# Kernel tuning notes

Hardware: AMD Instinct MI355X
Metric: run time of the kernel (lower is better)

## Reference

```python
import jax, jax.numpy as jnp
import numpy as np

DIM = 512
NUM_HEADS = 8
DIM_HEAD = DIM // NUM_HEADS


def _xavier(key, shape):
    fan_in, fan_out = shape[0], shape[1]
    a = (6.0 / (fan_in + fan_out)) ** 0.5
    return jax.random.uniform(key, shape, jnp.float32, -a, a)


def setup_inputs() -> dict:
    key = jax.random.key(0)
    ks = jax.random.split(key, 8)
    B, N, M = 2, 2048, 2048
    x = jax.random.normal(ks[0], (B, N, DIM), jnp.float32)
    source = jax.random.normal(ks[1], (B, M, DIM), jnp.float32)
    source_mask = jax.random.randint(ks[2], (B, M), 0, 2) > 0
    Wq = _xavier(ks[3], (DIM, DIM)); bq = jnp.zeros((DIM,), jnp.float32)
    Wk = _xavier(ks[4], (DIM, DIM)); bk = jnp.zeros((DIM,), jnp.float32)
    Wv = _xavier(ks[5], (DIM, DIM)); bv = jnp.zeros((DIM,), jnp.float32)
    Wm = _xavier(ks[6], (DIM, DIM)); bm = jnp.zeros((DIM,), jnp.float32)
    return {"x": x, "source": source, "source_mask": source_mask,
            "Wq": Wq, "bq": bq, "Wk": Wk, "bk": bk,
            "Wv": Wv, "bv": bv, "Wm": Wm, "bm": bm}


def reference(x, source, source_mask, Wq, bq, Wk, bk, Wv, bv, Wm, bm):
    B, N, D = x.shape
    M = source.shape[-2]
    H, Dh = NUM_HEADS, DIM_HEAD
    # projections (torch Linear: x @ W^T + b)
    q = (x @ Wq.T + bq).reshape(B, N, H, Dh)
    k = (source @ Wk.T + bk).reshape(B, M, H, Dh)
    v = (source @ Wv.T + bv).reshape(B, M, H, Dh)
    scale = 1.0 / (Dh ** 0.5)
    # scores: [B, N, M, H]
    scores = jnp.einsum('bnhd,bmhd->bnmh', q, k) * scale
    scores = jnp.where(source_mask[:, None, :, None], scores, -jnp.inf)
    prob = jax.nn.softmax(scores, axis=-2)  # softmax over m
    agg = jnp.einsum('bnmh,bmhd->bnhd', prob, v).reshape(B, N, D)
    return agg @ Wm.T + bm
```

## Files before the change

### kernel.cpp

```cpp
#include <hip/hip_runtime.h>
#include <hip/hip_bf16.h>

#define DIMF 512
#define NHEAD 8
#define DHEAD 64
#define BATCH 2
#define SEQN 2048
#define SEQM 2048
#define FPS 40
#define QSCALE 0.18033688011112042f

typedef unsigned short u16;
typedef __attribute__((ext_vector_type(8))) short bf16x8;
typedef __attribute__((ext_vector_type(4))) float f32x4;

static __device__ __forceinline__ u16 f2bf(float f) {
    unsigned u = __float_as_uint(f);
    u += 0x7FFF + ((u >> 16) & 1);
    return (u16)(u >> 16);
}

static __device__ __forceinline__
void load16(const u16* g, u16* l) {
    __builtin_amdgcn_global_load_lds(
        (const __attribute__((address_space(1))) void*)g,
        (__attribute__((address_space(3))) void*)l,
        16, 0, 0);
}

static __device__ __forceinline__
void permpair(unsigned& a, unsigned& c) {
#if __has_builtin(__builtin_amdgcn_permlane32_swap)
    {
        auto r1 = __builtin_amdgcn_permlane32_swap(a, c, false, false);
        unsigned a1 = r1[0], c1 = r1[1];
        auto r2 = __builtin_amdgcn_permlane16_swap(a1, c1, false, false);
        a = r2[0]; c = r2[1];
    }
#else
    asm("v_permlane32_swap_b32 %0, %1" : "+v"(a), "+v"(c));
    asm("v_permlane16_swap_b32 %0, %1" : "+v"(a), "+v"(c));
#endif
}

#define LDS_BARRIER() do {                                      \
    asm volatile("s_waitcnt lgkmcnt(0)" ::: "memory");          \
    __builtin_amdgcn_s_barrier();                               \
    __builtin_amdgcn_sched_barrier(0);                          \
} while (0)

__global__ __launch_bounds__(256)
void cvt_w(const float* __restrict__ wq, const float* __restrict__ wk,
           const float* __restrict__ wv, const float* __restrict__ wm,
           const int* __restrict__ mask,
           u16* __restrict__ wqb, u16* __restrict__ wkb,
           u16* __restrict__ wvb, u16* __restrict__ wmb,
           u16* __restrict__ maskbf)
{
    int i = (blockIdx.x * 256 + threadIdx.x) * 4;
    if (blockIdx.y == 4) {
        if (i < BATCH * SEQM) {
            int4 m4 = *(const int4*)&mask[i];
            *(ushort4*)&maskbf[i] = make_ushort4(m4.x ? 0x3F80 : 0, m4.y ? 0x3F80 : 0,
                                                 m4.z ? 0x3F80 : 0, m4.w ? 0x3F80 : 0);
        }
        return;
    }
    const float* in = (blockIdx.y == 0) ? wq : (blockIdx.y == 1) ? wk
                    : (blockIdx.y == 2) ? wv : wm;
    u16* out = (blockIdx.y == 0) ? wqb : (blockIdx.y == 1) ? wkb
             : (blockIdx.y == 2) ? wvb : wmb;
    if (i >= DIMF * DIMF) return;
    float4 v = *(const float4*)&in[i];
    *(ushort4*)&out[i] = make_ushort4(f2bf(v.x), f2bf(v.y), f2bf(v.z), f2bf(v.w));
}

#define ASZ (64 * FPS)
#define BSZ (128 * FPS)

__device__ __forceinline__
void gemm_mfma(const float* __restrict__ Xf, const u16* __restrict__ Xb,
               const u16* __restrict__ W, const float* __restrict__ bias,
               const int* __restrict__ msk, void* __restrict__ Out, int mode)
{
    __shared__ __align__(16) u16 SH[2 * ASZ + 2 * BSZ];

    const int tid  = threadIdx.x;
    const int wave = tid >> 6;
    const int lane = tid & 63;
    const int l15  = lane & 15;
    const int quad = lane >> 4;
    const int wm = wave & 1, wn = wave >> 1;
    const int r0 = blockIdx.x * 64, c0 = blockIdx.y * 128;

    f32x4 acc[2][4] = {};

    const int br = tid >> 2, boct = tid & 3;
    const int ar = tid >> 3, aseg = tid & 7;

    bf16x8 rb0, rb1, rab;
    float4 ra0, ra1;

    auto loadg = [&](int k0) {
        rb0 = *(const bf16x8*)&W[(size_t)(c0 + br) * DIMF + k0 + boct * 8];
        rb1 = *(const bf16x8*)&W[(size_t)(c0 + br + 64) * DIMF + k0 + boct * 8];
        if (Xf) {
            ra0 = *(const float4*)&Xf[(size_t)(r0 + ar) * DIMF + k0 + aseg * 4];
            ra1 = *(const float4*)&Xf[(size_t)(r0 + ar + 32) * DIMF + k0 + aseg * 4];
        } else {
            rab = *(const bf16x8*)&Xb[(size_t)(r0 + br) * DIMF + k0 + boct * 8];
        }
    };
    auto stage = [&](int buf) {
        u16* As = SH + buf * ASZ;
        u16* Bs = SH + 2 * ASZ + buf * BSZ;
        if (Xf) {
            *(ushort4*)&As[ar * FPS + aseg * 4] =
                make_ushort4(f2bf(ra0.x), f2bf(ra0.y), f2bf(ra0.z), f2bf(ra0.w));
            *(ushort4*)&As[(ar + 32) * FPS + aseg * 4] =
                make_ushort4(f2bf(ra1.x), f2bf(ra1.y), f2bf(ra1.z), f2bf(ra1.w));
        } else {
            *(bf16x8*)&As[br * FPS + boct * 8] = rab;
        }
        *(bf16x8*)&Bs[br * FPS + boct * 8] = rb0;
        *(bf16x8*)&Bs[(br + 64) * FPS + boct * 8] = rb1;
    };

    loadg(0);
    stage(0);
    loadg(32);
    LDS_BARRIER();

    const int NK = DIMF / 32;
    for (int kt = 0; kt < NK; ++kt) {
        const int cur = kt & 1;
        if (kt + 1 < NK) stage(cur ^ 1);
        if (kt + 2 < NK) loadg((kt + 2) * 32);
        const u16* As = SH + cur * ASZ;
        const u16* Bs = SH + 2 * ASZ + cur * BSZ;

        bf16x8 af[2], bf[4];
        #pragma unroll
        for (int mi = 0; mi < 2; ++mi)
            af[mi] = *(const bf16x8*)&As[(wm * 32 + mi * 16 + l15) * FPS + quad * 8];
        #pragma unroll
        for (int ni = 0; ni < 4; ++ni)
            bf[ni] = *(const bf16x8*)&Bs[(wn * 64 + ni * 16 + l15) * FPS + quad * 8];
        #pragma unroll
        for (int mi = 0; mi < 2; ++mi)
            #pragma unroll
            for (int ni = 0; ni < 4; ++ni)
                acc[mi][ni] = __builtin_amdgcn_mfma_f32_16x16x32_bf16(
                    af[mi], bf[ni], acc[mi][ni], 0, 0, 0);
        LDS_BARRIER();
    }

    float bb[4];
    #pragma unroll
    for (int ni = 0; ni < 4; ++ni)
        bb[ni] = bias[c0 + wn * 64 + ni * 16 + l15];

    if (mode == 2) {
        u16* T = SH;
        const int b = r0 >> 11;
        const int n_base = r0 & (SEQN - 1);
        #pragma unroll
        for (int hh = 0; hh < 2; ++hh) {
            __syncthreads();
            if (wn == hh) {
                #pragma unroll
                for (int mi = 0; mi < 2; ++mi) {
                    const int rl = wm * 32 + mi * 16 + quad * 4;
                    int4 m4 = *(const int4*)&msk[b * SEQM + n_base + rl];
                    float mm[4];
                    mm[0] = m4.x ? 1.f : 0.f; mm[1] = m4.y ? 1.f : 0.f;
                    mm[2] = m4.z ? 1.f : 0.f; mm[3] = m4.w ? 1.f : 0.f;
                    #pragma unroll
                    for (int ni = 0; ni < 4; ++ni)
                        #pragma unroll
                        for (int r = 0; r < 4; ++r)
                            T[(rl + r) * 72 + ni * 16 + l15] =
                                f2bf((acc[mi][ni][r] + bb[ni]) * mm[r]);
                }
            }
            __syncthreads();
            const int d = tid >> 2, ms = (tid & 3) << 4;
            u16 tmp[16];
            #pragma unroll
            for (int j = 0; j < 16; ++j) tmp[j] = T[(ms + j) * 72 + d];
            const int hgl = (c0 >> 6) + hh;
            u16* dst = (u16*)Out + ((size_t)(b * NHEAD + hgl) * DHEAD + d) * SEQM
                       + n_base + ms;
            *(bf16x8*)&dst[0] = *(bf16x8*)&tmp[0];
            *(bf16x8*)&dst[8] = *(bf16x8*)&tmp[8];
        }
        return;
    }

    #pragma unroll
    for (int mi = 0; mi < 2; ++mi) {
        const int Rbase = r0 + wm * 32 + mi * 16 + quad * 4;
        const int b = Rbase >> 11;
        const int nb = Rbase & (SEQN - 1);
        #pragma unroll
        for (int ni = 0; ni < 4; ++ni) {
            const int C = c0 + wn * 64 + ni * 16 + l15;
            const int h = C >> 6, d = C & 63;
            if (mode == 0) {
                u16* ow = (u16*)Out;
                #pragma unroll
                for (int r = 0; r < 4; ++r)
                    ow[(((size_t)(b * NHEAD + h) * SEQN) + nb + r) * DHEAD + d] =
                        f2bf((acc[mi][ni][r] + bb[ni]) * QSCALE);
            } else if (mode == 1) {
                u16* ow = (u16*)Out;
                #pragma unroll
                for (int r = 0; r < 4; ++r)
                    ow[(((size_t)(b * NHEAD + h) * SEQN) + nb + r) * DHEAD + d] =
                        f2bf(acc[mi][ni][r] + bb[ni]);
            } else {
                float* ow = (float*)Out;
                #pragma unroll
                for (int r = 0; r < 4; ++r)
                    ow[(size_t)(Rbase + r) * DIMF + C] = acc[mi][ni][r] + bb[ni];
            }
        }
    }
}

__global__ __launch_bounds__(256, 3)
void qkv_proj(const float* __restrict__ x, const float* __restrict__ src,
              const u16* __restrict__ wqb, const float* __restrict__ bq,
              const u16* __restrict__ wkb, const float* __restrict__ bk,
              const u16* __restrict__ wvb, const float* __restrict__ bv,
              const int* __restrict__ mask,
              u16* __restrict__ qw, u16* __restrict__ kw, u16* __restrict__ vtw)
{
    const int z = blockIdx.z;
    const float* X = (z == 0) ? x : src;
    const u16* W = (z == 0) ? wqb : (z == 1) ? wkb : wvb;
    const float* B = (z == 0) ? bq : (z == 1) ? bk : bv;
    void* O = (z == 0) ? (void*)qw : (z == 1) ? (void*)kw : (void*)vtw;
    gemm_mfma(X, nullptr, W, B, mask, O, z);
}

__global__ __launch_bounds__(256, 3)
void out_proj(const u16* __restrict__ aggb, const u16* __restrict__ wmb,
              const float* __restrict__ bm, float* __restrict__ out)
{
    gemm_mfma(nullptr, aggb, wmb, bm, nullptr, (void*)out, 3);
}

__global__ __launch_bounds__(256, 2)
void flash_attn_mfma(const u16* __restrict__ q, const u16* __restrict__ k,
                     const u16* __restrict__ vt, const u16* __restrict__ maskbf,
                     u16* __restrict__ agg)
{
    __shared__ __align__(16) u16 KsD[2][4096];
    __shared__ __align__(16) u16 VtsD[2][4096];
    float* Osum = (float*)&KsD[0][0];
    float* Lsum = (float*)&VtsD[0][0];

    const int tid  = threadIdx.x;
    const int wave = tid >> 6;
    const int lane = tid & 63;
    const int l15  = lane & 15;
    const int quad = lane >> 4;
    const int qg = wave >> 1, mh = wave & 1;

    const int bid  = blockIdx.x;
    const int xcd  = bid & 7, slot = bid >> 3;
    const int pair = (xcd << 1) | (slot & 1);
    const int b = pair >> 3, h = pair & 7;
    const int n0 = (slot >> 1) * 64;

    const size_t hoff = (size_t)(b * NHEAD + h) * (size_t)SEQM * DHEAD;
    const u16* kb = k  + hoff;
    const u16* vb = vt + hoff;
    const u16* mb = maskbf + b * SEQM;

    const int dr   = lane >> 3;
    const int doct = (lane & 7) ^ (dr & 7);
    const int g0 = wave, g1 = 4 + wave;
    const u16* kq0 = kb + (size_t)(g0 * 8 + dr) * DHEAD + doct * 8;
    const u16* kq1 = kb + (size_t)(g1 * 8 + dr) * DHEAD + doct * 8;
    const u16* vq0 = vb + (size_t)(g0 * 8 + dr) * SEQM + doct * 8;
    const u16* vq1 = vb + (size_t)(g1 * 8 + dr) * SEQM + doct * 8;

    bf16x8 qf[2][2];
    #pragma unroll
    for (int qh = 0; qh < 2; ++qh) {
        const u16* qp = q + hoff + (size_t)(n0 + qg * 32 + qh * 16 + l15) * DHEAD
                        + quad * 8;
        qf[qh][0] = *(const bf16x8*)qp;
        qf[qh][1] = *(const bf16x8*)(qp + 32);
    }

    load16(kq0, &KsD[0][g0 * 512]);
    load16(kq1, &KsD[0][g1 * 512]);
    load16(vq0, &VtsD[0][g0 * 512]);
    load16(vq1, &VtsD[0][g1 * 512]);
    bf16x8 mf_nxt = *(const bf16x8*)&mb[32 * mh + quad * 8];

    f32x4 O[2][4] = {};
    f32x4 lacc[2] = {};
    const int xoct = l15 & 7;

    for (int mt = 0; mt < SEQM / 64; ++mt) {
        const int cur = mt & 1;
        __syncthreads();
        bf16x8 mf = mf_nxt;
        if (mt + 1 < SEQM / 64) {
            const int m1 = (mt + 1) * 64;
            const int nb = cur ^ 1;
            load16(kq0 + (size_t)m1 * DHEAD, &KsD[nb][g0 * 512]);
            load16(kq1 + (size_t)m1 * DHEAD, &KsD[nb][g1 * 512]);
            load16(vq0 + m1, &VtsD[nb][g0 * 512]);
            load16(vq1 + m1, &VtsD[nb][g1 * 512]);
            mf_nxt = *(const bf16x8*)&mb[m1 + 32 * mh + quad * 8];
        }
        const u16* Ks  = KsD[cur];
        const u16* Vts = VtsD[cur];

        f32x4 st[2][2] = {};
        __builtin_amdgcn_s_setprio(1);
        #pragma unroll
        for (int sub = 0; sub < 2; ++sub) {
            const int mrow = 32 * mh + 16 * sub + l15;
            #pragma unroll
            for (int c = 0; c < 2; ++c) {
                const int oct = (4 * c + quad) ^ xoct;
                bf16x8 af = *(const bf16x8*)&Ks[mrow * 64 + oct * 8];
                #pragma unroll
                for (int qh = 0; qh < 2; ++qh)
                    st[qh][sub] = __builtin_amdgcn_mfma_f32_16x16x32_bf16(
                        af, qf[qh][c], st[qh][sub], 0, 0, 0);
            }
        }
        __builtin_amdgcn_s_setprio(0);

        bf16x8 pfr[2];
        #pragma unroll
        for (int qh = 0; qh < 2; ++qh) {
            float e00 = __builtin_amdgcn_exp2f(st[qh][0][0]);
            float e01 = __builtin_amdgcn_exp2f(st[qh][0][1]);
            float e02 = __builtin_amdgcn_exp2f(st[qh][0][2]);
            float e03 = __builtin_amdgcn_exp2f(st[qh][0][3]);
            float e10 = __builtin_amdgcn_exp2f(st[qh][1][0]);
            float e11 = __builtin_amdgcn_exp2f(st[qh][1][1]);
            float e12 = __builtin_amdgcn_exp2f(st[qh][1][2]);
            float e13 = __builtin_amdgcn_exp2f(st[qh][1][3]);
            unsigned a0, a1, c0w, c1w;
            asm("v_cvt_pk_bf16_f32 %0, %1, %2" : "=v"(a0)  : "v"(e00), "v"(e01));
            asm("v_cvt_pk_bf16_f32 %0, %1, %2" : "=v"(a1)  : "v"(e02), "v"(e03));
            asm("v_cvt_pk_bf16_f32 %0, %1, %2" : "=v"(c0w) : "v"(e10), "v"(e11));
            asm("v_cvt_pk_bf16_f32 %0, %1, %2" : "=v"(c1w) : "v"(e12), "v"(e13));
            permpair(a0, c0w);
            permpair(a1, c1w);
            union { unsigned u[4]; bf16x8 hv; } pu;
            pu.u[0] = a0; pu.u[1] = a1; pu.u[2] = c0w; pu.u[3] = c1w;
            pfr[qh] = pu.hv;
        }

        bf16x8 vf[4];
        #pragma unroll
        for (int sd = 0; sd < 4; ++sd) {
            const int oct = (4 * mh + quad) ^ xoct;
            vf[sd] = *(const bf16x8*)&Vts[(16 * sd + l15) * 64 + oct * 8];
        }

        __builtin_amdgcn_s_setprio(1);
        #pragma unroll
        for (int qh = 0; qh < 2; ++qh) {
            lacc[qh] = __builtin_amdgcn_mfma_f32_16x16x32_bf16(
                pfr[qh], mf, lacc[qh], 0, 0, 0);
            #pragma unroll
            for (int sd = 0; sd < 4; ++sd)
                O[qh][sd] = __builtin_amdgcn_mfma_f32_16x16x32_bf16(
                    pfr[qh], vf[sd], O[qh][sd], 0, 0, 0);
        }
        __builtin_amdgcn_s_setprio(0);
    }

    __syncthreads();
    if (mh == 1) {
        #pragma unroll
        for (int qh = 0; qh < 2; ++qh) {
            #pragma unroll
            for (int sd = 0; sd < 4; ++sd)
                #pragma unroll
                for (int r = 0; r < 4; ++r)
                    Osum[qg * 2048 + (qh * 16 + quad * 4 + r) * 64 + 16 * sd + l15]
                        = O[qh][sd][r];
            if (l15 == 0) {
                #pragma unroll
                for (int r = 0; r < 4; ++r)
                    Lsum[qg * 32 + qh * 16 + quad * 4 + r] = lacc[qh][r];
            }
        }
    }
    __syncthreads();
    if (mh == 0) {
        #pragma unroll
        for (int qh = 0; qh < 2; ++qh)
            #pragma unroll
            for (int r = 0; r < 4; ++r) {
                const float inv = 1.f /
                    (lacc[qh][r] + Lsum[qg * 32 + qh * 16 + quad * 4 + r]);
                const int n = n0 + qg * 32 + qh * 16 + quad * 4 + r;
                u16* ag = agg + ((size_t)b * SEQN + n) * DIMF + h * DHEAD + l15;
                #pragma unroll
                for (int sd = 0; sd < 4; ++sd)
                    ag[16 * sd] = f2bf((O[qh][sd][r] +
                        Osum[qg * 2048 + (qh * 16 + quad * 4 + r) * 64 + 16 * sd + l15])
                        * inv);
            }
    }
}

extern "C" void kernel_launch(void* const* d_in, const int* in_sizes, int n_in,
                              void* d_out, int out_size, void* d_ws, size_t ws_size,
                              hipStream_t stream)
{
    (void)in_sizes; (void)n_in; (void)out_size; (void)ws_size;
    const float* x      = (const float*)d_in[0];
    const float* source = (const float*)d_in[1];
    const int*   mask   = (const int*)  d_in[2];
    const float* Wq = (const float*)d_in[3]; const float* bq = (const float*)d_in[4];
    const float* Wk = (const float*)d_in[5]; const float* bk = (const float*)d_in[6];
    const float* Wv = (const float*)d_in[7]; const float* bv = (const float*)d_in[8];
    const float* Wm = (const float*)d_in[9]; const float* bm = (const float*)d_in[10];
    float* out = (float*)d_out;

    const size_t SZ = (size_t)BATCH * SEQN * DIMF;
    const size_t WZ = (size_t)DIMF * DIMF;
    u16* qw   = (u16*)d_ws;
    u16* kw   = qw  + SZ;
    u16* vtw  = kw  + SZ;
    u16* aggb = vtw + SZ;
    u16* wqb  = aggb + SZ;
    u16* wkb  = wqb + WZ;
    u16* wvb  = wkb + WZ;
    u16* wmb  = wvb + WZ;
    u16* maskbf = wmb + WZ;

    dim3 gcvt((WZ / 4 + 255) / 256, 5);
    cvt_w<<<gcvt, 256, 0, stream>>>(Wq, Wk, Wv, Wm, mask,
                                    wqb, wkb, wvb, wmb, maskbf);

    dim3 gproj(4096 / 64, 512 / 128, 3);
    qkv_proj<<<gproj, 256, 0, stream>>>(x, source, wqb, bq, wkb, bk, wvb, bv,
                                        mask, qw, kw, vtw);

    flash_attn_mfma<<<512, 256, 0, stream>>>(qw, kw, vtw, maskbf, aggb);

    dim3 gout(4096 / 64, 512 / 128);
    out_proj<<<gout, 256, 0, stream>>>(aggb, wmb, bm, out);
}
```

Before: 140.2 us.

## Split attention over key halves and merge partials inside output projection

The attention kernel now splits the key/value sequence into two halves, launching twice as many blocks. Each block writes an unnormalized fp32 partial output and its row sum. The output projection GEMM loads both partials, adds them, normalizes, and converts to bf16 while staging its A tile. The aim is more blocks to fill the GPU and fewer serial tile iterations per block, at the cost of extra fp32 partial traffic through global memory. The attention launch bound is also raised to 4 blocks per SM. The merge skips max-rescaling, so it appears to rely on the original kernel not using a running max, or on both halves sharing a fixed offset.

```diff
diff --git a/kernel.cpp b/kernel.cpp
--- a/kernel.cpp
+++ b/kernel.cpp
@@ -77,9 +77,12 @@
 
 #define ASZ (64 * FPS)
 #define BSZ (128 * FPS)
+#define PSZ ((size_t)BATCH * NHEAD * SEQN * DHEAD)
+#define LSZ ((size_t)BATCH * NHEAD * SEQN)
 
 __device__ __forceinline__
 void gemm_mfma(const float* __restrict__ Xf, const u16* __restrict__ Xb,
+               const float* __restrict__ Op, const float* __restrict__ lp,
                const u16* __restrict__ W, const float* __restrict__ bias,
                const int* __restrict__ msk, void* __restrict__ Out, int mode)
 {
@@ -99,7 +102,8 @@
     const int ar = tid >> 3, aseg = tid & 7;
 
     bf16x8 rb0, rb1, rab;
-    float4 ra0, ra1;
+    float4 ra0, ra1, ra0b, ra1b;
+    float l00, l01, l10, l11;
 
     auto loadg = [&](int k0) {
         rb0 = *(const bf16x8*)&W[(size_t)(c0 + br) * DIMF + k0 + boct * 8];
@@ -107,6 +111,20 @@
         if (Xf) {
             ra0 = *(const float4*)&Xf[(size_t)(r0 + ar) * DIMF + k0 + aseg * 4];
             ra1 = *(const float4*)&Xf[(size_t)(r0 + ar + 32) * DIMF + k0 + aseg * 4];
+        } else if (Op) {
+            const int D = k0 + aseg * 4, hD = D >> 6, dD = D & 63;
+            const int Ra = r0 + ar, ba = Ra >> 11, na = Ra & (SEQN - 1);
+            const int Rb = Ra + 32, bb_ = Rb >> 11, nb_ = Rb & (SEQN - 1);
+            const size_t pa = (((size_t)ba * NHEAD + hD) * SEQN + na) * DHEAD + dD;
+            const size_t pb = (((size_t)bb_ * NHEAD + hD) * SEQN + nb_) * DHEAD + dD;
+            ra0  = *(const float4*)&Op[pa];
+            ra0b = *(const float4*)&Op[pa + PSZ];
+            ra1  = *(const float4*)&Op[pb];
+            ra1b = *(const float4*)&Op[pb + PSZ];
+            const size_t la = ((size_t)ba * NHEAD + hD) * SEQN + na;
+            const size_t lb = ((size_t)bb_ * NHEAD + hD) * SEQN + nb_;
+            l00 = lp[la]; l01 = lp[la + LSZ];
+            l10 = lp[lb]; l11 = lp[lb + LSZ];
         } else {
             rab = *(const bf16x8*)&Xb[(size_t)(r0 + br) * DIMF + k0 + boct * 8];
         }
@@ -119,6 +137,15 @@
                 make_ushort4(f2bf(ra0.x), f2bf(ra0.y), f2bf(ra0.z), f2bf(ra0.w));
             *(ushort4*)&As[(ar + 32) * FPS + aseg * 4] =
                 make_ushort4(f2bf(ra1.x), f2bf(ra1.y), f2bf(ra1.z), f2bf(ra1.w));
+        } else if (Op) {
+            const float inv0 = __builtin_amdgcn_rcpf(l00 + l01);
+            const float inv1 = __builtin_amdgcn_rcpf(l10 + l11);
+            *(ushort4*)&As[ar * FPS + aseg * 4] = make_ushort4(
+                f2bf((ra0.x + ra0b.x) * inv0), f2bf((ra0.y + ra0b.y) * inv0),
+                f2bf((ra0.z + ra0b.z) * inv0), f2bf((ra0.w + ra0b.w) * inv0));
+            *(ushort4*)&As[(ar + 32) * FPS + aseg * 4] = make_ushort4(
+                f2bf((ra1.x + ra1b.x) * inv1), f2bf((ra1.y + ra1b.y) * inv1),
+                f2bf((ra1.z + ra1b.z) * inv1), f2bf((ra1.w + ra1b.w) * inv1));
         } else {
             *(bf16x8*)&As[br * FPS + boct * 8] = rab;
         }
@@ -241,20 +268,21 @@
     const u16* W = (z == 0) ? wqb : (z == 1) ? wkb : wvb;
     const float* B = (z == 0) ? bq : (z == 1) ? bk : bv;
     void* O = (z == 0) ? (void*)qw : (z == 1) ? (void*)kw : (void*)vtw;
-    gemm_mfma(X, nullptr, W, B, mask, O, z);
+    gemm_mfma(X, nullptr, nullptr, nullptr, W, B, mask, O, z);
 }
 
 __global__ __launch_bounds__(256, 3)
-void out_proj(const u16* __restrict__ aggb, const u16* __restrict__ wmb,
-              const float* __restrict__ bm, float* __restrict__ out)
-{
-    gemm_mfma(nullptr, aggb, wmb, bm, nullptr, (void*)out, 3);
-}
-
-__global__ __launch_bounds__(256, 2)
+void out_proj(const float* __restrict__ Opart, const float* __restrict__ lpart,
+              const u16* __restrict__ wmb, const float* __restrict__ bm,
+              float* __restrict__ out)
+{
+    gemm_mfma(nullptr, nullptr, Opart, lpart, wmb, bm, nullptr, (void*)out, 3);
+}
+
+__global__ __launch_bounds__(256, 4)
 void flash_attn_mfma(const u16* __restrict__ q, const u16* __restrict__ k,
                      const u16* __restrict__ vt, const u16* __restrict__ maskbf,
-                     u16* __restrict__ agg)
+                     float* __restrict__ Opart, float* __restrict__ lpart)
 {
     __shared__ __align__(16) u16 KsD[2][4096];
     __shared__ __align__(16) u16 VtsD[2][4096];
@@ -270,22 +298,24 @@
 
     const int bid  = blockIdx.x;
     const int xcd  = bid & 7, slot = bid >> 3;
+    const int s    = slot >> 6;
     const int pair = (xcd << 1) | (slot & 1);
     const int b = pair >> 3, h = pair & 7;
-    const int n0 = (slot >> 1) * 64;
+    const int n0 = ((slot >> 1) & 31) * 64;
+    const int m0 = s * (SEQM / 2);
 
     const size_t hoff = (size_t)(b * NHEAD + h) * (size_t)SEQM * DHEAD;
     const u16* kb = k  + hoff;
     const u16* vb = vt + hoff;
-    const u16* mb = maskbf + b * SEQM;
+    const u16* mbs = maskbf + b * SEQM + m0;
 
     const int dr   = lane >> 3;
     const int doct = (lane & 7) ^ (dr & 7);
     const int g0 = wave, g1 = 4 + wave;
-    const u16* kq0 = kb + (size_t)(g0 * 8 + dr) * DHEAD + doct * 8;
-    const u16* kq1 = kb + (size_t)(g1 * 8 + dr) * DHEAD + doct * 8;
-    const u16* vq0 = vb + (size_t)(g0 * 8 + dr) * SEQM + doct * 8;
-    const u16* vq1 = vb + (size_t)(g1 * 8 + dr) * SEQM + doct * 8;
+    const u16* kq0 = kb + (size_t)(m0 + g0 * 8 + dr) * DHEAD + doct * 8;
+    const u16* kq1 = kb + (size_t)(m0 + g1 * 8 + dr) * DHEAD + doct * 8;
+    const u16* vq0 = vb + (size_t)(g0 * 8 + dr) * SEQM + m0 + doct * 8;
+    const u16* vq1 = vb + (size_t)(g1 * 8 + dr) * SEQM + m0 + doct * 8;
 
     bf16x8 qf[2][2];
     #pragma unroll
@@ -300,24 +330,25 @@
     load16(kq1, &KsD[0][g1 * 512]);
     load16(vq0, &VtsD[0][g0 * 512]);
     load16(vq1, &VtsD[0][g1 * 512]);
-    bf16x8 mf_nxt = *(const bf16x8*)&mb[32 * mh + quad * 8];
+    bf16x8 mf_nxt = *(const bf16x8*)&mbs[32 * mh + quad * 8];
 
     f32x4 O[2][4] = {};
     f32x4 lacc[2] = {};
     const int xoct = l15 & 7;
-
-    for (int mt = 0; mt < SEQM / 64; ++mt) {
+    const int NT = (SEQM / 2) / 64;
+
+    for (int mt = 0; mt < NT; ++mt) {
         const int cur = mt & 1;
         __syncthreads();
         bf16x8 mf = mf_nxt;
-        if (mt + 1 < SEQM / 64) {
+        if (mt + 1 < NT) {
             const int m1 = (mt + 1) * 64;
             const int nb = cur ^ 1;
             load16(kq0 + (size_t)m1 * DHEAD, &KsD[nb][g0 * 512]);
             load16(kq1 + (size_t)m1 * DHEAD, &KsD[nb][g1 * 512]);
             load16(vq0 + m1, &VtsD[nb][g0 * 512]);
             load16(vq1 + m1, &VtsD[nb][g1 * 512]);
-            mf_nxt = *(const bf16x8*)&mb[m1 + 32 * mh + quad * 8];
+            mf_nxt = *(const bf16x8*)&mbs[m1 + 32 * mh + quad * 8];
         }
         const u16* Ks  = KsD[cur];
         const u16* Vts = VtsD[cur];
@@ -405,15 +436,16 @@
         for (int qh = 0; qh < 2; ++qh)
             #pragma unroll
             for (int r = 0; r < 4; ++r) {
-                const float inv = 1.f /
-                    (lacc[qh][r] + Lsum[qg * 32 + qh * 16 + quad * 4 + r]);
-                const int n = n0 + qg * 32 + qh * 16 + quad * 4 + r;
-                u16* ag = agg + ((size_t)b * SEQN + n) * DIMF + h * DHEAD + l15;
+                const int rr = qh * 16 + quad * 4 + r;
+                const float lsum = lacc[qh][r] + Lsum[qg * 32 + rr];
+                const int n = n0 + qg * 32 + rr;
+                float* Og = Opart + (size_t)s * PSZ
+                          + (((size_t)(b * NHEAD + h)) * SEQN + n) * DHEAD + l15;
                 #pragma unroll
                 for (int sd = 0; sd < 4; ++sd)
-                    ag[16 * sd] = f2bf((O[qh][sd][r] +
-                        Osum[qg * 2048 + (qh * 16 + quad * 4 + r) * 64 + 16 * sd + l15])
-                        * inv);
+                    Og[16 * sd] = O[qh][sd][r] + Osum[qg * 2048 + rr * 64 + 16 * sd + l15];
+                if (l15 == 0)
+                    lpart[(size_t)s * LSZ + ((size_t)(b * NHEAD + h)) * SEQN + n] = lsum;
             }
     }
 }
@@ -437,12 +469,13 @@
     u16* qw   = (u16*)d_ws;
     u16* kw   = qw  + SZ;
     u16* vtw  = kw  + SZ;
-    u16* aggb = vtw + SZ;
-    u16* wqb  = aggb + SZ;
+    u16* wqb  = vtw + SZ;
     u16* wkb  = wqb + WZ;
     u16* wvb  = wkb + WZ;
     u16* wmb  = wvb + WZ;
     u16* maskbf = wmb + WZ;
+    float* Opart = (float*)(maskbf + (size_t)BATCH * SEQM);
+    float* lpart = Opart + 2 * PSZ;
 
     dim3 gcvt((WZ / 4 + 255) / 256, 5);
     cvt_w<<<gcvt, 256, 0, stream>>>(Wq, Wk, Wv, Wm, mask,
@@ -452,8 +485,8 @@
     qkv_proj<<<gproj, 256, 0, stream>>>(x, source, wqb, bq, wkb, bk, wvb, bv,
                                         mask, qw, kw, vtw);
 
-    flash_attn_mfma<<<512, 256, 0, stream>>>(qw, kw, vtw, maskbf, aggb);
+    flash_attn_mfma<<<1024, 256, 0, stream>>>(qw, kw, vtw, maskbf, Opart, lpart);
 
     dim3 gout(4096 / 64, 512 / 128);
-    out_proj<<<gout, 256, 0, stream>>>(aggb, wmb, bm, out);
-}
+    out_proj<<<gout, 256, 0, stream>>>(Opart, lpart, wmb, bm, out);
+}
```

Measured after the change: 145.3 us. 1.04x slower.

## Load K/V tiles directly into registers, replacing LDS double buffering

Applied to the files above, without the earlier changes.

The flash attention loop no longer stages K and V tiles through LDS with global_load_lds and per-tile barriers. Each wave now loads its own MFMA operand fragments straight from global memory into registers, using a two-tile register ping-pong for prefetch. This removes the __syncthreads and LDS traffic from the main loop. In exchange, K/V data that waves used to share through LDS is now fetched redundantly from global/L2, loads are less coalesced, and register pressure rises, which may reduce occupancy.

```diff
diff --git a/kernel.cpp b/kernel.cpp
--- a/kernel.cpp
+++ b/kernel.cpp
@@ -18,14 +18,6 @@
     unsigned u = __float_as_uint(f);
     u += 0x7FFF + ((u >> 16) & 1);
     return (u16)(u >> 16);
-}
-
-static __device__ __forceinline__
-void load16(const u16* g, u16* l) {
-    __builtin_amdgcn_global_load_lds(
-        (const __attribute__((address_space(1))) void*)g,
-        (__attribute__((address_space(3))) void*)l,
-        16, 0, 0);
 }
 
 static __device__ __forceinline__
@@ -256,10 +248,8 @@
                      const u16* __restrict__ vt, const u16* __restrict__ maskbf,
                      u16* __restrict__ agg)
 {
-    __shared__ __align__(16) u16 KsD[2][4096];
-    __shared__ __align__(16) u16 VtsD[2][4096];
-    float* Osum = (float*)&KsD[0][0];
-    float* Lsum = (float*)&VtsD[0][0];
+    __shared__ __align__(16) float Osum[4096];
+    __shared__ float Lsum[64];
 
     const int tid  = threadIdx.x;
     const int wave = tid >> 6;
@@ -279,13 +269,9 @@
     const u16* vb = vt + hoff;
     const u16* mb = maskbf + b * SEQM;
 
-    const int dr   = lane >> 3;
-    const int doct = (lane & 7) ^ (dr & 7);
-    const int g0 = wave, g1 = 4 + wave;
-    const u16* kq0 = kb + (size_t)(g0 * 8 + dr) * DHEAD + doct * 8;
-    const u16* kq1 = kb + (size_t)(g1 * 8 + dr) * DHEAD + doct * 8;
-    const u16* vq0 = vb + (size_t)(g0 * 8 + dr) * SEQM + doct * 8;
-    const u16* vq1 = vb + (size_t)(g1 * 8 + dr) * SEQM + doct * 8;
+    const u16* kw0 = kb + (size_t)(32 * mh + l15) * DHEAD + quad * 8;
+    const u16* vw0 = vb + (size_t)l15 * SEQM + (4 * mh + quad) * 8;
+    const u16* mw0 = mb + 32 * mh + quad * 8;
 
     bf16x8 qf[2][2];
     #pragma unroll
@@ -296,47 +282,34 @@
         qf[qh][1] = *(const bf16x8*)(qp + 32);
     }
 
-    load16(kq0, &KsD[0][g0 * 512]);
-    load16(kq1, &KsD[0][g1 * 512]);
-    load16(vq0, &VtsD[0][g0 * 512]);
-    load16(vq1, &VtsD[0][g1 * 512]);
-    bf16x8 mf_nxt = *(const bf16x8*)&mb[32 * mh + quad * 8];
-
     f32x4 O[2][4] = {};
     f32x4 lacc[2] = {};
-    const int xoct = l15 & 7;
-
-    for (int mt = 0; mt < SEQM / 64; ++mt) {
-        const int cur = mt & 1;
-        __syncthreads();
-        bf16x8 mf = mf_nxt;
-        if (mt + 1 < SEQM / 64) {
-            const int m1 = (mt + 1) * 64;
-            const int nb = cur ^ 1;
-            load16(kq0 + (size_t)m1 * DHEAD, &KsD[nb][g0 * 512]);
-            load16(kq1 + (size_t)m1 * DHEAD, &KsD[nb][g1 * 512]);
-            load16(vq0 + m1, &VtsD[nb][g0 * 512]);
-            load16(vq1 + m1, &VtsD[nb][g1 * 512]);
-            mf_nxt = *(const bf16x8*)&mb[m1 + 32 * mh + quad * 8];
-        }
-        const u16* Ks  = KsD[cur];
-        const u16* Vts = VtsD[cur];
-
+
+    auto loadTile = [&](int mt, bf16x8* af, bf16x8* vf, bf16x8& mf) {
+        const size_t moff = (size_t)mt * 64;
+        #pragma unroll
+        for (int sub = 0; sub < 2; ++sub)
+            #pragma unroll
+            for (int c = 0; c < 2; ++c)
+                af[sub * 2 + c] = *(const bf16x8*)
+                    (kw0 + (moff + 16 * sub) * DHEAD + c * 32);
+        #pragma unroll
+        for (int sd = 0; sd < 4; ++sd)
+            vf[sd] = *(const bf16x8*)(vw0 + (size_t)(16 * sd) * SEQM + moff);
+        mf = *(const bf16x8*)(mw0 + moff);
+    };
+
+    auto compute = [&](const bf16x8* af, const bf16x8* vf, bf16x8 mf) {
         f32x4 st[2][2] = {};
         __builtin_amdgcn_s_setprio(1);
         #pragma unroll
-        for (int sub = 0; sub < 2; ++sub) {
-            const int mrow = 32 * mh + 16 * sub + l15;
-            #pragma unroll
-            for (int c = 0; c < 2; ++c) {
-                const int oct = (4 * c + quad) ^ xoct;
-                bf16x8 af = *(const bf16x8*)&Ks[mrow * 64 + oct * 8];
+        for (int sub = 0; sub < 2; ++sub)
+            #pragma unroll
+            for (int c = 0; c < 2; ++c)
                 #pragma unroll
                 for (int qh = 0; qh < 2; ++qh)
                     st[qh][sub] = __builtin_amdgcn_mfma_f32_16x16x32_bf16(
-                        af, qf[qh][c], st[qh][sub], 0, 0, 0);
-            }
-        }
+                        af[sub * 2 + c], qf[qh][c], st[qh][sub], 0, 0, 0);
         __builtin_amdgcn_s_setprio(0);
 
         bf16x8 pfr[2];
@@ -362,13 +335,6 @@
             pfr[qh] = pu.hv;
         }
 
-        bf16x8 vf[4];
-        #pragma unroll
-        for (int sd = 0; sd < 4; ++sd) {
-            const int oct = (4 * mh + quad) ^ xoct;
-            vf[sd] = *(const bf16x8*)&Vts[(16 * sd + l15) * 64 + oct * 8];
-        }
-
         __builtin_amdgcn_s_setprio(1);
         #pragma unroll
         for (int qh = 0; qh < 2; ++qh) {
@@ -380,6 +346,17 @@
                     pfr[qh], vf[sd], O[qh][sd], 0, 0, 0);
         }
         __builtin_amdgcn_s_setprio(0);
+    };
+
+    const int NT = SEQM / 64;
+    bf16x8 afA[4], vfA[4], mfA;
+    bf16x8 afB[4], vfB[4], mfB;
+    loadTile(0, afA, vfA, mfA);
+    for (int mt = 0; mt < NT; mt += 2) {
+        loadTile(mt + 1, afB, vfB, mfB);
+        compute(afA, vfA, mfA);
+        if (mt + 2 < NT) loadTile(mt + 2, afA, vfA, mfA);
+        compute(afB, vfB, mfB);
     }
 
     __syncthreads();
```

Result: slower. 175.9 us (+25.5%).

## Double attention key tile to 128 rows per iteration with new V swizzle

Applied to the files above, without the earlier changes.

The flash attention loop now processes 128 keys per iteration instead of 64, doubling the K and V LDS tiles and the per-wave score tile. This halves the number of barriers and loop iterations, so more MFMA work sits between synchronisations. V tiles now use a 128-wide layout with a 16-way XOR swizzle, and the exp/pack code moves into a helper. In exchange, LDS use per block doubles and register pressure grows, which may reduce occupancy at the declared two blocks per CU.

```diff
diff --git a/kernel.cpp b/kernel.cpp
--- a/kernel.cpp
+++ b/kernel.cpp
@@ -41,6 +41,28 @@
     asm("v_permlane32_swap_b32 %0, %1" : "+v"(a), "+v"(c));
     asm("v_permlane16_swap_b32 %0, %1" : "+v"(a), "+v"(c));
 #endif
+}
+
+static __device__ __forceinline__
+bf16x8 t12pack(f32x4 s0, f32x4 s1) {
+    float e00 = __builtin_amdgcn_exp2f(s0[0]);
+    float e01 = __builtin_amdgcn_exp2f(s0[1]);
+    float e02 = __builtin_amdgcn_exp2f(s0[2]);
+    float e03 = __builtin_amdgcn_exp2f(s0[3]);
+    float e10 = __builtin_amdgcn_exp2f(s1[0]);
+    float e11 = __builtin_amdgcn_exp2f(s1[1]);
+    float e12 = __builtin_amdgcn_exp2f(s1[2]);
+    float e13 = __builtin_amdgcn_exp2f(s1[3]);
+    unsigned a0, a1, c0w, c1w;
+    asm("v_cvt_pk_bf16_f32 %0, %1, %2" : "=v"(a0)  : "v"(e00), "v"(e01));
+    asm("v_cvt_pk_bf16_f32 %0, %1, %2" : "=v"(a1)  : "v"(e02), "v"(e03));
+    asm("v_cvt_pk_bf16_f32 %0, %1, %2" : "=v"(c0w) : "v"(e10), "v"(e11));
+    asm("v_cvt_pk_bf16_f32 %0, %1, %2" : "=v"(c1w) : "v"(e12), "v"(e13));
+    permpair(a0, c0w);
+    permpair(a1, c1w);
+    union { unsigned u[4]; bf16x8 hv; } pu;
+    pu.u[0] = a0; pu.u[1] = a1; pu.u[2] = c0w; pu.u[3] = c1w;
+    return pu.hv;
 }
 
 #define LDS_BARRIER() do {                                      \
@@ -256,8 +278,8 @@
                      const u16* __restrict__ vt, const u16* __restrict__ maskbf,
                      u16* __restrict__ agg)
 {
-    __shared__ __align__(16) u16 KsD[2][4096];
-    __shared__ __align__(16) u16 VtsD[2][4096];
+    __shared__ __align__(16) u16 KsD[2][8192];
+    __shared__ __align__(16) u16 VtsD[2][8192];
     float* Osum = (float*)&KsD[0][0];
     float* Lsum = (float*)&VtsD[0][0];
 
@@ -279,13 +301,18 @@
     const u16* vb = vt + hoff;
     const u16* mb = maskbf + b * SEQM;
 
-    const int dr   = lane >> 3;
-    const int doct = (lane & 7) ^ (dr & 7);
-    const int g0 = wave, g1 = 4 + wave;
-    const u16* kq0 = kb + (size_t)(g0 * 8 + dr) * DHEAD + doct * 8;
-    const u16* kq1 = kb + (size_t)(g1 * 8 + dr) * DHEAD + doct * 8;
-    const u16* vq0 = vb + (size_t)(g0 * 8 + dr) * SEQM + doct * 8;
-    const u16* vq1 = vb + (size_t)(g1 * 8 + dr) * SEQM + doct * 8;
+    const int dr  = lane >> 3;
+    const int kct = (lane & 7) ^ (dr & 7);
+    const int vr  = lane >> 4;
+    const int vct = (lane & 15) ^ ((4 * wave + vr) & 15);
+    const u16* kq[4];
+    const u16* vq[4];
+    #pragma unroll
+    for (int j = 0; j < 4; ++j) {
+        const int g = wave + 4 * j;
+        kq[j] = kb + (size_t)(g * 8 + dr) * DHEAD + kct * 8;
+        vq[j] = vb + (size_t)(g * 4 + vr) * SEQM + vct * 8;
+    }
 
     bf16x8 qf[2][2];
     #pragma unroll
@@ -296,40 +323,44 @@
         qf[qh][1] = *(const bf16x8*)(qp + 32);
     }
 
-    load16(kq0, &KsD[0][g0 * 512]);
-    load16(kq1, &KsD[0][g1 * 512]);
-    load16(vq0, &VtsD[0][g0 * 512]);
-    load16(vq1, &VtsD[0][g1 * 512]);
-    bf16x8 mf_nxt = *(const bf16x8*)&mb[32 * mh + quad * 8];
+    #pragma unroll
+    for (int j = 0; j < 4; ++j) {
+        load16(kq[j], &KsD[0][(wave + 4 * j) * 512]);
+        load16(vq[j], &VtsD[0][(wave + 4 * j) * 512]);
+    }
+    bf16x8 mfA_nxt = *(const bf16x8*)&mb[64 * mh + quad * 8];
+    bf16x8 mfB_nxt = *(const bf16x8*)&mb[64 * mh + 32 + quad * 8];
 
     f32x4 O[2][4] = {};
     f32x4 lacc[2] = {};
-    const int xoct = l15 & 7;
-
-    for (int mt = 0; mt < SEQM / 64; ++mt) {
+    const int NT = SEQM / 128;
+
+    for (int mt = 0; mt < NT; ++mt) {
         const int cur = mt & 1;
         __syncthreads();
-        bf16x8 mf = mf_nxt;
-        if (mt + 1 < SEQM / 64) {
-            const int m1 = (mt + 1) * 64;
+        bf16x8 mfA = mfA_nxt, mfB = mfB_nxt;
+        if (mt + 1 < NT) {
+            const size_t m1 = (size_t)(mt + 1) * 128;
             const int nb = cur ^ 1;
-            load16(kq0 + (size_t)m1 * DHEAD, &KsD[nb][g0 * 512]);
-            load16(kq1 + (size_t)m1 * DHEAD, &KsD[nb][g1 * 512]);
-            load16(vq0 + m1, &VtsD[nb][g0 * 512]);
-            load16(vq1 + m1, &VtsD[nb][g1 * 512]);
-            mf_nxt = *(const bf16x8*)&mb[m1 + 32 * mh + quad * 8];
+            #pragma unroll
+            for (int j = 0; j < 4; ++j) {
+                load16(kq[j] + m1 * DHEAD, &KsD[nb][(wave + 4 * j) * 512]);
+                load16(vq[j] + m1, &VtsD[nb][(wave + 4 * j) * 512]);
+            }
+            mfA_nxt = *(const bf16x8*)&mb[m1 + 64 * mh + quad * 8];
+            mfB_nxt = *(const bf16x8*)&mb[m1 + 64 * mh + 32 + quad * 8];
         }
         const u16* Ks  = KsD[cur];
         const u16* Vts = VtsD[cur];
 
-        f32x4 st[2][2] = {};
+        f32x4 st[2][4] = {};
         __builtin_amdgcn_s_setprio(1);
         #pragma unroll
-        for (int sub = 0; sub < 2; ++sub) {
-            const int mrow = 32 * mh + 16 * sub + l15;
+        for (int sub = 0; sub < 4; ++sub) {
+            const int mrow = 64 * mh + 16 * sub + l15;
             #pragma unroll
             for (int c = 0; c < 2; ++c) {
-                const int oct = (4 * c + quad) ^ xoct;
+                const int oct = (4 * c + quad) ^ (l15 & 7);
                 bf16x8 af = *(const bf16x8*)&Ks[mrow * 64 + oct * 8];
                 #pragma unroll
                 for (int qh = 0; qh < 2; ++qh)
@@ -339,45 +370,34 @@
         }
         __builtin_amdgcn_s_setprio(0);
 
-        bf16x8 pfr[2];
+        bf16x8 pfrA[2], pfrB[2];
         #pragma unroll
         for (int qh = 0; qh < 2; ++qh) {
-            float e00 = __builtin_amdgcn_exp2f(st[qh][0][0]);
-            float e01 = __builtin_amdgcn_exp2f(st[qh][0][1]);
-            float e02 = __builtin_amdgcn_exp2f(st[qh][0][2]);
-            float e03 = __builtin_amdgcn_exp2f(st[qh][0][3]);
-            float e10 = __builtin_amdgcn_exp2f(st[qh][1][0]);
-            float e11 = __builtin_amdgcn_exp2f(st[qh][1][1]);
-            float e12 = __builtin_amdgcn_exp2f(st[qh][1][2]);
-            float e13 = __builtin_amdgcn_exp2f(st[qh][1][3]);
-            unsigned a0, a1, c0w, c1w;
-            asm("v_cvt_pk_bf16_f32 %0, %1, %2" : "=v"(a0)  : "v"(e00), "v"(e01));
-            asm("v_cvt_pk_bf16_f32 %0, %1, %2" : "=v"(a1)  : "v"(e02), "v"(e03));
-            asm("v_cvt_pk_bf16_f32 %0, %1, %2" : "=v"(c0w) : "v"(e10), "v"(e11));
-            asm("v_cvt_pk_bf16_f32 %0, %1, %2" : "=v"(c1w) : "v"(e12), "v"(e13));
-            permpair(a0, c0w);
-            permpair(a1, c1w);
-            union { unsigned u[4]; bf16x8 hv; } pu;
-            pu.u[0] = a0; pu.u[1] = a1; pu.u[2] = c0w; pu.u[3] = c1w;
-            pfr[qh] = pu.hv;
-        }
-
-        bf16x8 vf[4];
-        #pragma unroll
-        for (int sd = 0; sd < 4; ++sd) {
-            const int oct = (4 * mh + quad) ^ xoct;
-            vf[sd] = *(const bf16x8*)&Vts[(16 * sd + l15) * 64 + oct * 8];
+            pfrA[qh] = t12pack(st[qh][0], st[qh][1]);
+            pfrB[qh] = t12pack(st[qh][2], st[qh][3]);
         }
 
         __builtin_amdgcn_s_setprio(1);
         #pragma unroll
         for (int qh = 0; qh < 2; ++qh) {
             lacc[qh] = __builtin_amdgcn_mfma_f32_16x16x32_bf16(
-                pfr[qh], mf, lacc[qh], 0, 0, 0);
-            #pragma unroll
-            for (int sd = 0; sd < 4; ++sd)
+                pfrA[qh], mfA, lacc[qh], 0, 0, 0);
+            lacc[qh] = __builtin_amdgcn_mfma_f32_16x16x32_bf16(
+                pfrB[qh], mfB, lacc[qh], 0, 0, 0);
+        }
+        #pragma unroll
+        for (int sd = 0; sd < 4; ++sd) {
+            const int pA = (8 * mh + quad) ^ l15;
+            const int pB = (8 * mh + 4 + quad) ^ l15;
+            bf16x8 vfA = *(const bf16x8*)&Vts[(16 * sd + l15) * 128 + pA * 8];
+            bf16x8 vfB = *(const bf16x8*)&Vts[(16 * sd + l15) * 128 + pB * 8];
+            #pragma unroll
+            for (int qh = 0; qh < 2; ++qh) {
                 O[qh][sd] = __builtin_amdgcn_mfma_f32_16x16x32_bf16(
-                    pfr[qh], vf[sd], O[qh][sd], 0, 0, 0);
+                    pfrA[qh], vfA, O[qh][sd], 0, 0, 0);
+                O[qh][sd] = __builtin_amdgcn_mfma_f32_16x16x32_bf16(
+                    pfrB[qh], vfB, O[qh][sd], 0, 0, 0);
+            }
         }
         __builtin_amdgcn_s_setprio(0);
     }
```

After: 137.0 us (median of 2 runs). 1.02x faster.
